# Kernel tuning notes

Hardware: AMD Instinct MI355X
Metric: run time of the kernel (lower is better)

Reference implementation:

```python
import jax, jax.numpy as jnp
import numpy as np

N_VIEWS, N_JOINTS, HM_H, HM_W = 5, 15, 128, 240
P = 4
VX = VY = VZ = 64
FX = FY = 253
FZ = 64
WHOLE_SIZE = np.array([8000.0, 8000.0, 2000.0], np.float32)
CENTER = np.array([0.0, -500.0, 800.0], np.float32)
IND_SIZE = np.array([2000.0, 2000.0, 2000.0], np.float32)
FINE = np.array([FX, FY, FZ], np.float32)


def setup_inputs() -> dict:
    key = jax.random.key(0)
    k1, k2, k3, k4 = jax.random.split(key, 4)
    heatmaps = jax.random.uniform(k1, (N_VIEWS, N_JOINTS, HM_H, HM_W), jnp.float32)
    # cached per-view fine-voxel sampling grid, clamped to [-1.1, 1.1] as in project_grid
    sample_grids = jax.random.uniform(k2, (N_VIEWS, FX, FY, FZ, 2), jnp.float32) * 2.2 - 1.1
    xyz = jnp.asarray(CENTER) + (jax.random.uniform(k3, (P, 3), jnp.float32) - 0.5) * jnp.asarray(WHOLE_SIZE - IND_SIZE)
    wh = jax.random.uniform(k4, (P, 2), jnp.float32, minval=0.2, maxval=1.0)
    proposal_centers = jnp.concatenate([xyz, jnp.zeros((P, 2), jnp.float32), wh], axis=1)
    return {"heatmaps": heatmaps, "sample_grids": sample_grids, "proposal_centers": proposal_centers}


def _grid_sample_2d(img, gx, gy):
    # img: [J,H,W]; gx,gy: [...]  bilinear, align_corners=True, zero padding (torch defaults)
    H, W = img.shape[-2:]
    px = (gx + 1.0) * 0.5 * (W - 1)
    py = (gy + 1.0) * 0.5 * (H - 1)
    x0 = jnp.floor(px)
    y0 = jnp.floor(py)
    wx1 = px - x0
    wy1 = py - y0

    def pick(xi, yi):
        ok = ((xi >= 0) & (xi < W) & (yi >= 0) & (yi < H)).astype(img.dtype)
        xc = jnp.clip(xi, 0, W - 1).astype(jnp.int32)
        yc = jnp.clip(yi, 0, H - 1).astype(jnp.int32)
        return img[:, yc, xc] * ok  # [J, ...]

    return (pick(x0, y0) * ((1 - wx1) * (1 - wy1))
            + pick(x0 + 1, y0) * (wx1 * (1 - wy1))
            + pick(x0, y0 + 1) * ((1 - wx1) * wy1)
            + pick(x0 + 1, y0 + 1) * (wx1 * wy1))


def _grids():
    # self.grids: computed once from INDIVIDUAL space size around whole-space center
    gx = np.linspace(-IND_SIZE[0] / 2, IND_SIZE[0] / 2, VX) + CENTER[0]
    gy = np.linspace(-IND_SIZE[1] / 2, IND_SIZE[1] / 2, VY) + CENTER[1]
    gz = np.linspace(-IND_SIZE[2] / 2, IND_SIZE[2] / 2, VZ) + CENTER[2]
    grid = np.stack(np.meshgrid(gx, gy, gz, indexing='ij'), axis=-1)  # [VX,VY,VZ,3]
    grids = np.stack([grid[:, :, 0, :2].reshape(-1, 2),
                      grid[:, 0, :, ::2].reshape(-1, 2),
                      grid[0, :, :, 1:].reshape(-1, 2)])
    return jnp.asarray(grids, jnp.float32)


def _forward(heatmaps, sample_grids, proposal_centers):
    pc = jax.lax.stop_gradient(proposal_centers)  # index math is non-differentiable
    mask_x = jnp.maximum(((1.0 - pc[:, 5]) / 2.0 * (VX - 1)).astype(jnp.int32), 0)
    mask_y = jnp.maximum(((1.0 - pc[:, 6]) / 2.0 * (VY - 1)).astype(jnp.int32), 0)
    ctl = jnp.round((pc[:, 0:3] + jnp.asarray(WHOLE_SIZE) / 2.0 - jnp.asarray(CENTER)
                     - jnp.asarray(IND_SIZE) / 2.0) / jnp.asarray(WHOLE_SIZE)
                    * (jnp.asarray(FINE) - 1.0)).astype(jnp.int32)
    x, y, z = ctl[:, 0], ctl[:, 1], ctl[:, 2]
    x_start = jnp.maximum(-x, 0) + mask_x
    x_end = jnp.minimum(FX - x, VX) - mask_x
    y_start = jnp.maximum(-y, 0) + mask_y
    y_end = jnp.minimum(FY - y, VY) - mask_y
    z_start = jnp.maximum(-z, 0)
    z_end = jnp.minimum(FZ - z, VZ)

    ix = jnp.arange(VX)
    iy = jnp.arange(VY)
    iz = jnp.arange(VZ)
    vx = (ix[None, :] >= x_start[:, None]) & (ix[None, :] < x_end[:, None])  # [P,VX]
    vy = (iy[None, :] >= y_start[:, None]) & (iy[None, :] < y_end[:, None])
    vz = (iz[None, :] >= z_start[:, None]) & (iz[None, :] < z_end[:, None])
    valid = vx[:, :, None, None] & vy[:, None, :, None] & vz[:, None, None, :]  # [P,VX,VY,VZ]

    # fine-grid indices for every output voxel (clipped; invalid ones masked out)
    fx = jnp.clip(x[:, None] + ix[None, :], 0, FX - 1)  # [P,VX]
    fy = jnp.clip(y[:, None] + iy[None, :], 0, FY - 1)
    fz = jnp.clip(z[:, None] + iz[None, :], 0, FZ - 1)
    sg = sample_grids[:, fx[:, :, None, None], fy[:, None, :, None], fz[:, None, None, :], :]  # [n,P,VX,VY,VZ,2]

    sampled = jax.vmap(_grid_sample_2d)(heatmaps, sg[..., 0], sg[..., 1])  # [n,J,P,VX,VY,VZ]
    cubes = jnp.mean(sampled, axis=0).transpose(1, 0, 2, 3, 4)  # [P,J,VX,VY,VZ]
    cubes = jnp.clip(cubes * valid[:, None, :, :, :].astype(cubes.dtype), 0.0, 1.0)
    return cubes


def reference(heatmaps, sample_grids, proposal_centers):
    cubes = _forward(heatmaps, sample_grids, proposal_centers)
    return (cubes, _grids())
```

## Files before the change

### kernel.cpp

```cpp
#include <hip/hip_runtime.h>

#define N_VIEWS 5
#define N_JOINTS 15
#define HM_H 128
#define HM_W 240
#define PB 4
#define VXn 64
#define VYn 64
#define VZn 64
#define FXn 253
#define FYn 253
#define FZn 64
#define JP 16

typedef float        vf2 __attribute__((ext_vector_type(2)));
typedef unsigned int vu4 __attribute__((ext_vector_type(4)));

#define T_TOTAL (N_VIEWS * HM_H * HM_W)
#define G_TOTAL (3 * 4096)

__global__ void prep_kernel(const float* __restrict__ hm,
                            unsigned char* __restrict__ T,
                            float* __restrict__ gout) {
    int t = blockIdx.x * blockDim.x + threadIdx.x;
    if (t < T_TOTAL) {
        int x = t % HM_W;
        int vy = t / HM_W;
        int y = vy % HM_H;
        int v = vy / HM_H;
        unsigned int w[4] = {0u, 0u, 0u, 0u};
#pragma unroll
        for (int j = 0; j < N_JOINTS; ++j) {
            float val = hm[(((size_t)v * N_JOINTS + j) * HM_H + y) * HM_W + x];
            float q = rintf(val * 255.0f);
            q = fminf(fmaxf(q, 0.0f), 255.0f);
            w[j >> 2] |= ((unsigned int)q) << ((j & 3) * 8);
        }
        vu4* dst = (vu4*)(T + (size_t)t * JP);
        vu4 o; o.x = w[0]; o.y = w[1]; o.z = w[2]; o.w = w[3];
        *dst = o;
    } else {
        int u = t - T_TOTAL;
        if (u >= G_TOTAL) return;
        int g = u / 4096;
        int idx = u % 4096;
        int a = idx / 64;
        int b = idx % 64;
        const float step = 2000.0f / 63.0f;
        float va = -1000.0f + (float)a * step;
        float vb = -1000.0f + (float)b * step;
        float o0, o1;
        if (g == 0)      { o0 = va + 0.0f;      o1 = vb + (-500.0f); }
        else if (g == 1) { o0 = va + 0.0f;      o1 = vb + 800.0f;    }
        else             { o0 = va + (-500.0f); o1 = vb + 800.0f;    }
        gout[(size_t)u * 2 + 0] = o0;
        gout[(size_t)u * 2 + 1] = o1;
    }
}

__global__ __launch_bounds__(256, 3) void project_kernel(
    const unsigned char* __restrict__ hmT,
    const float* __restrict__ sg,
    const float* __restrict__ pc,
    float* __restrict__ out)
{
    const int iz = threadIdx.x;
    const int iy = blockIdx.x * 4 + threadIdx.y;
    const int ix = blockIdx.y;
    const int p  = blockIdx.z;

    const float pw = pc[p * 7 + 5];
    const float ph = pc[p * 7 + 6];
    int mask_x = max((int)((1.0f - pw) / 2.0f * (float)(VXn - 1)), 0);
    int mask_y = max((int)((1.0f - ph) / 2.0f * (float)(VYn - 1)), 0);

    float tx = pc[p * 7 + 0] + 4000.0f; tx = tx - 0.0f;      tx = tx - 1000.0f;
    float ty = pc[p * 7 + 1] + 4000.0f; ty = ty - (-500.0f); ty = ty - 1000.0f;
    float tz = pc[p * 7 + 2] + 1000.0f; tz = tz - 800.0f;    tz = tz - 1000.0f;
    tx = tx / 8000.0f * 252.0f;
    ty = ty / 8000.0f * 252.0f;
    tz = tz / 2000.0f * 63.0f;
    int cx = (int)rintf(tx);
    int cy = (int)rintf(ty);
    int cz = (int)rintf(tz);

    int x_start = max(-cx, 0) + mask_x;
    int x_end   = min(FXn - cx, VXn) - mask_x;
    int y_start = max(-cy, 0) + mask_y;
    int y_end   = min(FYn - cy, VYn) - mask_y;
    int z_start = max(-cz, 0);
    int z_end   = min(FZn - cz, VZn);

    const bool valid = (ix >= x_start && ix < x_end) &&
                       (iy >= y_start && iy < y_end) &&
                       (iz >= z_start && iz < z_end);

    const size_t out_base = ((((size_t)p * N_JOINTS) * VXn + ix) * VYn + iy) * VZn + iz;
    const size_t out_jstride = (size_t)VXn * VYn * VZn;

    unsigned long long mv = __ballot(valid ? 1 : 0);
    if (mv == 0ull) {
#pragma unroll
        for (int j = 0; j < N_JOINTS; ++j)
            __builtin_nontemporal_store(0.0f, &out[out_base + j * out_jstride]);
        return;
    }

    const int fx = min(max(cx + ix, 0), FXn - 1);
    const int fy = min(max(cy + iy, 0), FYn - 1);
    const int fz = min(max(cz + iz, 0), FZn - 1);

    const size_t sg_base = (((size_t)fx * FYn + fy) * FZn + fz) * 2;
    const size_t sg_vstride = (size_t)FXn * FYn * FZn * 2;

    vf2 g[N_VIEWS];
#pragma unroll
    for (int v = 0; v < N_VIEWS; ++v)
        g[v] = __builtin_nontemporal_load(
            (const vf2*)(sg + sg_base + (size_t)v * sg_vstride));

    float w00[N_VIEWS], w10[N_VIEWS], w01[N_VIEWS], w11[N_VIEWS];
    unsigned off00[N_VIEWS], off10[N_VIEWS], off01[N_VIEWS], off11[N_VIEWS];
#pragma unroll
    for (int v = 0; v < N_VIEWS; ++v) {
        float px = (g[v].x + 1.0f) * 0.5f * (float)(HM_W - 1);
        float py = (g[v].y + 1.0f) * 0.5f * (float)(HM_H - 1);
        float x0f = floorf(px), y0f = floorf(py);
        float wx1 = px - x0f,  wy1 = py - y0f;
        float wx0 = 1.0f - wx1, wy0 = 1.0f - wy1;
        float x1f = x0f + 1.0f, y1f = y0f + 1.0f;
        float okx0 = (x0f >= 0.0f && x0f < (float)HM_W) ? 1.0f : 0.0f;
        float okx1 = (x1f >= 0.0f && x1f < (float)HM_W) ? 1.0f : 0.0f;
        float oky0 = (y0f >= 0.0f && y0f < (float)HM_H) ? 1.0f : 0.0f;
        float oky1 = (y1f >= 0.0f && y1f < (float)HM_H) ? 1.0f : 0.0f;
        int x0 = min(max((int)x0f, 0), HM_W - 1);
        int x1 = min(max((int)x0f + 1, 0), HM_W - 1);
        int y0 = min(max((int)y0f, 0), HM_H - 1);
        int y1 = min(max((int)y0f + 1, 0), HM_H - 1);
        w00[v] = wx0 * wy0 * okx0 * oky0;
        w10[v] = wx1 * wy0 * okx1 * oky0;
        w01[v] = wx0 * wy1 * okx0 * oky1;
        w11[v] = wx1 * wy1 * okx1 * oky1;
        unsigned vbase = (unsigned)(v * HM_H * HM_W);
        off00[v] = (vbase + (unsigned)y0 * HM_W + (unsigned)x0) * JP;
        off10[v] = (vbase + (unsigned)y0 * HM_W + (unsigned)x1) * JP;
        off01[v] = (vbase + (unsigned)y1 * HM_W + (unsigned)x0) * JP;
        off11[v] = (vbase + (unsigned)y1 * HM_W + (unsigned)x1) * JP;
    }

    vu4 tap[N_VIEWS][4];
#pragma unroll
    for (int v = 0; v < N_VIEWS; ++v) {
        tap[v][0] = *(const vu4*)(hmT + off00[v]);
        tap[v][1] = *(const vu4*)(hmT + off10[v]);
        tap[v][2] = *(const vu4*)(hmT + off01[v]);
        tap[v][3] = *(const vu4*)(hmT + off11[v]);
    }

    float acc[N_JOINTS];
#pragma unroll
    for (int j = 0; j < N_JOINTS; ++j) acc[j] = 0.0f;

#pragma unroll
    for (int v = 0; v < N_VIEWS; ++v) {
        const unsigned int* a = (const unsigned int*)&tap[v][0];
        const unsigned int* b = (const unsigned int*)&tap[v][1];
        const unsigned int* c = (const unsigned int*)&tap[v][2];
        const unsigned int* d = (const unsigned int*)&tap[v][3];
#pragma unroll
        for (int j = 0; j < N_JOINTS; ++j) {
            int word = j >> 2, sh = (j & 3) * 8;
            float fa = (float)((a[word] >> sh) & 0xffu);
            float fb = (float)((b[word] >> sh) & 0xffu);
            float fc = (float)((c[word] >> sh) & 0xffu);
            float fd = (float)((d[word] >> sh) & 0xffu);
            acc[j] += w00[v] * fa + w10[v] * fb + w01[v] * fc + w11[v] * fd;
        }
    }

    const float scale = valid ? (0.2f / 255.0f) : 0.0f;
#pragma unroll
    for (int j = 0; j < N_JOINTS; ++j) {
        float vlu = acc[j] * scale;
        vlu = fminf(fmaxf(vlu, 0.0f), 1.0f);
        __builtin_nontemporal_store(vlu, &out[out_base + j * out_jstride]);
    }
}

extern "C" void kernel_launch(void* const* d_in, const int* in_sizes, int n_in,
                              void* d_out, int out_size, void* d_ws, size_t ws_size,
                              hipStream_t stream) {
    const float* hm = (const float*)d_in[0];
    const float* sg = (const float*)d_in[1];
    const float* pc = (const float*)d_in[2];
    float* out = (float*)d_out;

    unsigned char* T = (unsigned char*)d_ws;

    const size_t grids_off = (size_t)PB * N_JOINTS * VXn * VYn * VZn;
    const int prep_total = T_TOTAL + G_TOTAL;
    prep_kernel<<<(prep_total + 255) / 256, 256, 0, stream>>>(hm, T, out + grids_off);

    dim3 blk(64, 4, 1);
    dim3 grd(16, 64, 4);
    project_kernel<<<grd, blk, 0, stream>>>(T, sg, pc, out);
}
```

Baseline: 66.06 us.

## Shrink project blocks to 128 threads, drop nontemporal hints, interleave tap loads

Changes the projection kernel from 256-thread 2D blocks to 128-thread 1D blocks, doubles the grid, and relaxes the launch bounds so the compiler is no longer held to three blocks per CU. Replaces nontemporal loads and stores with ordinary ones. Issues the heatmap tap loads inside the weight-computation loop rather than in a separate loop. These aim to improve scheduling and occupancy and let output writes use the cache normally, at the risk of higher register pressure and more cache pollution.

```diff
diff --git a/kernel.cpp b/kernel.cpp
--- a/kernel.cpp
+++ b/kernel.cpp
@@ -58,14 +58,14 @@
     }
 }
 
-__global__ __launch_bounds__(256, 3) void project_kernel(
+__global__ __launch_bounds__(128) void project_kernel(
     const unsigned char* __restrict__ hmT,
     const float* __restrict__ sg,
     const float* __restrict__ pc,
     float* __restrict__ out)
 {
-    const int iz = threadIdx.x;
-    const int iy = blockIdx.x * 4 + threadIdx.y;
+    const int iz = threadIdx.x & 63;
+    const int iy = blockIdx.x * 2 + (threadIdx.x >> 6);
     const int ix = blockIdx.y;
     const int p  = blockIdx.z;
 
@@ -102,7 +102,7 @@
     if (mv == 0ull) {
 #pragma unroll
         for (int j = 0; j < N_JOINTS; ++j)
-            __builtin_nontemporal_store(0.0f, &out[out_base + j * out_jstride]);
+            out[out_base + j * out_jstride] = 0.0f;
         return;
     }
 
@@ -116,11 +116,14 @@
     vf2 g[N_VIEWS];
 #pragma unroll
     for (int v = 0; v < N_VIEWS; ++v)
-        g[v] = __builtin_nontemporal_load(
-            (const vf2*)(sg + sg_base + (size_t)v * sg_vstride));
+        g[v] = *(const vf2*)(sg + sg_base + (size_t)v * sg_vstride);
+
+    float acc[N_JOINTS];
+#pragma unroll
+    for (int j = 0; j < N_JOINTS; ++j) acc[j] = 0.0f;
 
     float w00[N_VIEWS], w10[N_VIEWS], w01[N_VIEWS], w11[N_VIEWS];
-    unsigned off00[N_VIEWS], off10[N_VIEWS], off01[N_VIEWS], off11[N_VIEWS];
+    vu4 tap[N_VIEWS][4];
 #pragma unroll
     for (int v = 0; v < N_VIEWS; ++v) {
         float px = (g[v].x + 1.0f) * 0.5f * (float)(HM_W - 1);
@@ -142,36 +145,24 @@
         w01[v] = wx0 * wy1 * okx0 * oky1;
         w11[v] = wx1 * wy1 * okx1 * oky1;
         unsigned vbase = (unsigned)(v * HM_H * HM_W);
-        off00[v] = (vbase + (unsigned)y0 * HM_W + (unsigned)x0) * JP;
-        off10[v] = (vbase + (unsigned)y0 * HM_W + (unsigned)x1) * JP;
-        off01[v] = (vbase + (unsigned)y1 * HM_W + (unsigned)x0) * JP;
-        off11[v] = (vbase + (unsigned)y1 * HM_W + (unsigned)x1) * JP;
+        const unsigned char* base = hmT;
+        tap[v][0] = *(const vu4*)(base + (size_t)(vbase + (unsigned)y0 * HM_W + (unsigned)x0) * JP);
+        tap[v][1] = *(const vu4*)(base + (size_t)(vbase + (unsigned)y0 * HM_W + (unsigned)x1) * JP);
+        tap[v][2] = *(const vu4*)(base + (size_t)(vbase + (unsigned)y1 * HM_W + (unsigned)x0) * JP);
+        tap[v][3] = *(const vu4*)(base + (size_t)(vbase + (unsigned)y1 * HM_W + (unsigned)x1) * JP);
     }
-
-    vu4 tap[N_VIEWS][4];
-#pragma unroll
-    for (int v = 0; v < N_VIEWS; ++v) {
-        tap[v][0] = *(const vu4*)(hmT + off00[v]);
-        tap[v][1] = *(const vu4*)(hmT + off10[v]);
-        tap[v][2] = *(const vu4*)(hmT + off01[v]);
-        tap[v][3] = *(const vu4*)(hmT + off11[v]);
-    }
-
-    float acc[N_JOINTS];
-#pragma unroll
-    for (int j = 0; j < N_JOINTS; ++j) acc[j] = 0.0f;
 
 #pragma unroll
     for (int v = 0; v < N_VIEWS; ++v) {
         const unsigned int* a = (const unsigned int*)&tap[v][0];
-        const unsigned int* b = (const unsigned int*)&tap[v][1];
+        const unsigned int* bb = (const unsigned int*)&tap[v][1];
         const unsigned int* c = (const unsigned int*)&tap[v][2];
         const unsigned int* d = (const unsigned int*)&tap[v][3];
 #pragma unroll
         for (int j = 0; j < N_JOINTS; ++j) {
             int word = j >> 2, sh = (j & 3) * 8;
             float fa = (float)((a[word] >> sh) & 0xffu);
-            float fb = (float)((b[word] >> sh) & 0xffu);
+            float fb = (float)((bb[word] >> sh) & 0xffu);
             float fc = (float)((c[word] >> sh) & 0xffu);
             float fd = (float)((d[word] >> sh) & 0xffu);
             acc[j] += w00[v] * fa + w10[v] * fb + w01[v] * fc + w11[v] * fd;
@@ -183,7 +174,7 @@
     for (int j = 0; j < N_JOINTS; ++j) {
         float vlu = acc[j] * scale;
         vlu = fminf(fmaxf(vlu, 0.0f), 1.0f);
-        __builtin_nontemporal_store(vlu, &out[out_base + j * out_jstride]);
+        out[out_base + j * out_jstride] = vlu;
     }
 }
 
@@ -201,7 +192,7 @@
     const int prep_total = T_TOTAL + G_TOTAL;
     prep_kernel<<<(prep_total + 255) / 256, 256, 0, stream>>>(hm, T, out + grids_off);
 
-    dim3 blk(64, 4, 1);
-    dim3 grd(16, 64, 4);
+    dim3 blk(128, 1, 1);
+    dim3 grd(32, 64, 4);
     project_kernel<<<grd, blk, 0, stream>>>(T, sg, pc, out);
 }
```

Measured after the change: 65.94 us. About the same (-0.2%).
